# Optimization experiments

Hardware: AMD Instinct MI355X
Metric: run time of the kernel (lower is better)

Reference implementation:

```python
import jax, jax.numpy as jnp
import numpy as np

N_NODES = 50000
N_EDGES = 600000
DIM_H = 128
LN_EPS = 1e-5


def setup_inputs() -> dict:
    key = jax.random.key(0)
    ks = jax.random.split(key, 8)
    s = 1.0 / np.sqrt(DIM_H)
    return {
        "nodes": jax.random.normal(ks[0], (N_NODES, DIM_H), jnp.float32),
        "W_msg": jax.random.normal(ks[1], (DIM_H, DIM_H), jnp.float32) * s,
        "b_msg": jnp.zeros((DIM_H,), jnp.float32),
        "w_ih": jax.random.normal(ks[2], (3 * DIM_H, DIM_H), jnp.float32) * s,
        "w_hh": jax.random.normal(ks[3], (3 * DIM_H, DIM_H), jnp.float32) * s,
        "b_ih": jnp.zeros((3 * DIM_H,), jnp.float32),
        "b_hh": jnp.zeros((3 * DIM_H,), jnp.float32),
        "ln_gamma": jnp.ones((DIM_H,), jnp.float32),
        "ln_beta": jnp.zeros((DIM_H,), jnp.float32),
        "edge_src": jax.random.randint(ks[4], (N_EDGES,), 0, N_NODES, jnp.int32),
        "edge_dst": jax.random.randint(ks[5], (N_EDGES,), 0, N_NODES, jnp.int32),
    }


def _layer_norm(x, gamma, beta):
    mu = jnp.mean(x, axis=-1, keepdims=True)
    var = jnp.mean(jnp.square(x - mu), axis=-1, keepdims=True)
    return gamma * (x - mu) * jax.lax.rsqrt(var + LN_EPS) + beta


def reference(nodes, W_msg, b_msg, w_ih, w_hh, b_ih, b_hh, ln_gamma, ln_beta,
              edge_src, edge_dst):
    n_nodes = nodes.shape[0]
    # send_and_recv: per-edge message from source node, sum-reduce at dest
    msg_e = nodes[edge_src] @ W_msg.T + b_msg            # [E, H] (irregular gather)
    messages = jax.ops.segment_sum(msg_e, edge_dst, num_segments=n_nodes)  # [N, H]
    # global connection: add mean node feature
    msg = messages + jnp.mean(nodes, axis=0)
    # single-step GRU (torch gate layout: r, z, n)
    gi = msg @ w_ih.T + b_ih                             # [N, 3H]
    gh = nodes @ w_hh.T + b_hh                           # [N, 3H]
    i_r, i_z, i_n = jnp.split(gi, 3, axis=-1)
    h_r, h_z, h_n = jnp.split(gh, 3, axis=-1)
    r = jax.nn.sigmoid(i_r + h_r)
    z = jax.nn.sigmoid(i_z + h_z)
    n = jnp.tanh(i_n + r * h_n)
    h_next = (1.0 - z) * n + z * nodes
    # LayerNorm then post-GRU spatial residual with messages
    out = _layer_norm(h_next, ln_gamma, ln_beta)
    out = out + messages
    return out
```

## Files before the change

kernel.cpp:

```cpp
#include <hip/hip_runtime.h>
#include <hip/hip_bf16.h>

#define N_NODES 50000
#define N_EDGES 600000
#define DIM_H   128
#define NPAD    50048
#define NB_SCAN 196

typedef __attribute__((ext_vector_type(8))) short bf16x8;
typedef __attribute__((ext_vector_type(4))) float f32x4;
typedef __attribute__((ext_vector_type(4))) short short4v;

__device__ __forceinline__ short f2bs(float f) {
    __hip_bfloat16 h = __float2bfloat16(f);
    return *reinterpret_cast<short*>(&h);
}
__device__ __forceinline__ float bs2f(short s) {
    unsigned u = ((unsigned)(unsigned short)s) << 16;
    return __builtin_bit_cast(float, u);
}
__device__ __forceinline__ float sigm(float x) { return 1.f / (1.f + expf(-x)); }

__device__ __forceinline__ void dma16(const void* g, const void* lds_uniform) {
    __builtin_amdgcn_global_load_lds(
        (const __attribute__((address_space(1))) void*)g,
        (__attribute__((address_space(3))) void*)(unsigned)(unsigned long long)lds_uniform,
        16, 0, 0);
}

__global__ __launch_bounds__(256) void prep_k(const float* __restrict__ wmsg,
                                              const float* __restrict__ wih,
                                              const float* __restrict__ whh,
                                              short* __restrict__ wmsgB,
                                              short* __restrict__ wihB,
                                              short* __restrict__ whhB,
                                              int* __restrict__ cnt,
                                              float* __restrict__ colsum,
                                              short* __restrict__ aggTail,
                                              short* __restrict__ nodesTail,
                                              short* __restrict__ msginTail) {
    int i = blockIdx.x * 256 + threadIdx.x;
    if (i < 16384) wmsgB[i] = f2bs(wmsg[i]);
    if (i < 49152) { wihB[i] = f2bs(wih[i]); whhB[i] = f2bs(whh[i]); }
    if (i < N_NODES) cnt[i] = 0;
    if (i < 128) colsum[i] = 0.f;
    if (i < 1536) {
        short4v z = {0, 0, 0, 0};
        *(short4v*)(aggTail   + i * 4) = z;
        *(short4v*)(nodesTail + i * 4) = z;
        *(short4v*)(msginTail + i * 4) = z;
    }
}

__global__ __launch_bounds__(256) void colsum_k(const float* __restrict__ nodes,
                                                float* __restrict__ colsum,
                                                short* __restrict__ nodesB) {
    __shared__ float red[8][128];
    const int tid = threadIdx.x;
    const int cg = tid & 31;
    const int rl = tid >> 5;
    float4 acc = {0.f, 0.f, 0.f, 0.f};
    for (int r = blockIdx.x * 8 + rl; r < N_NODES; r += gridDim.x * 8) {
        float4 v = *(const float4*)(nodes + (size_t)r * DIM_H + cg * 4);
        acc.x += v.x; acc.y += v.y; acc.z += v.z; acc.w += v.w;
        *(short4v*)(nodesB + (size_t)r * DIM_H + cg * 4) =
            (short4v){f2bs(v.x), f2bs(v.y), f2bs(v.z), f2bs(v.w)};
    }
    *(float4*)&red[rl][cg * 4] = acc;
    __syncthreads();
    if (tid < 128) {
        float s = 0.f;
#pragma unroll
        for (int i = 0; i < 8; ++i) s += red[i][tid];
        unsafeAtomicAdd(&colsum[tid], s);
    }
}

__global__ __launch_bounds__(256) void hist_k(const int* __restrict__ edst,
                                              int* __restrict__ cnt) {
    int e = blockIdx.x * 256 + threadIdx.x;
    if (e < N_EDGES) atomicAdd(&cnt[edst[e]], 1);
}

__global__ __launch_bounds__(256) void bsum_k(const int* __restrict__ cnt,
                                              int* __restrict__ bsum) {
    const int t = threadIdx.x;
    int i = blockIdx.x * 256 + t;
    int v = (i < N_NODES) ? cnt[i] : 0;
#pragma unroll
    for (int o = 32; o; o >>= 1) v += __shfl_xor(v, o, 64);
    __shared__ int w4[4];
    if ((t & 63) == 0) w4[t >> 6] = v;
    __syncthreads();
    if (t == 0) bsum[blockIdx.x] = w4[0] + w4[1] + w4[2] + w4[3];
}

__global__ __launch_bounds__(256) void scan2_k(const int* __restrict__ cnt,
                                               const int* __restrict__ bsum,
                                               int* __restrict__ rowptr,
                                               int* __restrict__ pos) {
    const int b = blockIdx.x, t = threadIdx.x;
    const int lane = t & 63, w = t >> 6;
    __shared__ int red[4];
    __shared__ int wsum[4];

    int ov = (t < b) ? bsum[t] : 0;
#pragma unroll
    for (int o = 32; o; o >>= 1) ov += __shfl_xor(ov, o, 64);
    if (lane == 0) red[w] = ov;
    __syncthreads();
    const int offset = red[0] + red[1] + red[2] + red[3];

    int i = b * 256 + t;
    int v = (i < N_NODES) ? cnt[i] : 0;
    int x = v;
#pragma unroll
    for (int o = 1; o < 64; o <<= 1) {
        int y = __shfl_up(x, o, 64);
        if (lane >= o) x += y;
    }
    if (lane == 63) wsum[w] = x;
    __syncthreads();
    int woff = 0;
#pragma unroll
    for (int j = 0; j < 4; ++j)
        if (j < w) woff += wsum[j];
    int excl = offset + woff + (x - v);
    if (i < N_NODES) { rowptr[i] = excl; pos[i] = excl; }
    if (i == N_NODES - 1) rowptr[N_NODES] = excl + v;
}

__global__ __launch_bounds__(256) void reorder_k(const int* __restrict__ esrc,
                                                 const int* __restrict__ edst,
                                                 int* __restrict__ pos,
                                                 int* __restrict__ ssrc) {
    int e = blockIdx.x * 256 + threadIdx.x;
    if (e < N_EDGES) {
        int p = atomicAdd(&pos[edst[e]], 1);
        ssrc[p] = esrc[e];
    }
}

__global__ __launch_bounds__(256) void aggregate_k(const short* __restrict__ nodesB,
                                                   const int* __restrict__ rowptr,
                                                   const int* __restrict__ ssrc,
                                                   short* __restrict__ aggB) {
    const int wid = threadIdx.x >> 6;
    const int lane = threadIdx.x & 63;
    const int n = blockIdx.x * 4 + wid;
    if (n >= N_NODES) return;
    const int s0 = rowptr[n], s1 = rowptr[n + 1];
    float2 acc = {0.f, 0.f};
    int e = s0;
    for (; e + 3 < s1; e += 4) {
        int sa = ssrc[e], sb = ssrc[e + 1], sc = ssrc[e + 2], sd = ssrc[e + 3];
        short2 va = ((const short2*)(nodesB + (size_t)sa * DIM_H))[lane];
        short2 vb = ((const short2*)(nodesB + (size_t)sb * DIM_H))[lane];
        short2 vc = ((const short2*)(nodesB + (size_t)sc * DIM_H))[lane];
        short2 vd = ((const short2*)(nodesB + (size_t)sd * DIM_H))[lane];
        acc.x += (bs2f(va.x) + bs2f(vb.x)) + (bs2f(vc.x) + bs2f(vd.x));
        acc.y += (bs2f(va.y) + bs2f(vb.y)) + (bs2f(vc.y) + bs2f(vd.y));
    }
    for (; e < s1; ++e) {
        int sa = ssrc[e];
        short2 va = ((const short2*)(nodesB + (size_t)sa * DIM_H))[lane];
        acc.x += bs2f(va.x);
        acc.y += bs2f(va.y);
    }
    short2 o; o.x = f2bs(acc.x); o.y = f2bs(acc.y);
    ((short2*)(aggB + (size_t)n * DIM_H))[lane] = o;
}

__device__ __forceinline__ void stage_tile(const short* __restrict__ src, int row0,
                                           short* lds, int w, int lane) {
#pragma unroll
    for (int it = 0; it < 8; ++it) {
        int c = w * 8 + it;
        int s = c * 64 + lane;
        int r = s >> 4, q = s & 15;
        int g = q ^ (r & 15);
        dma16(src + (((size_t)(row0 + r)) << 7) + (g << 3), lds + (size_t)c * 512);
    }
}

__device__ __forceinline__ void wave_mm(const short* __restrict__ A,
                                        const short* __restrict__ W,
                                        f32x4 (&acc)[4][4],
                                        int wm, int wn, int r16, int half) {
#pragma unroll
    for (int kt = 0; kt < 4; ++kt) {
        const int sq = ((kt * 4 + half) ^ r16) << 3;
        bf16x8 af[4], bfr[4];
#pragma unroll
        for (int t = 0; t < 4; ++t) {
            af[t]  = *(const bf16x8*)&A[(wm + t * 16 + r16) * 128 + sq];
            bfr[t] = *(const bf16x8*)&W[(wn + t * 16 + r16) * 128 + sq];
        }
#pragma unroll
        for (int i = 0; i < 4; ++i)
#pragma unroll
            for (int j = 0; j < 4; ++j)
                acc[i][j] = __builtin_amdgcn_mfma_f32_16x16x32_bf16(
                    af[i], bfr[j], acc[i][j], 0, 0, 0);
    }
}

__global__ __launch_bounds__(256) void mgemm0_k(const short* __restrict__ aggB,
                                                const short* __restrict__ wmsgB,
                                                const float* __restrict__ bmsg,
                                                const int* __restrict__ degi,
                                                const float* __restrict__ colsum,
                                                short* __restrict__ msginB) {
    __shared__ short As[128 * 128];
    __shared__ short Ws[128 * 128];
    const int tid = threadIdx.x;
    const int lane = tid & 63, w = tid >> 6;
    const int m0 = blockIdx.x * 128;

    stage_tile(aggB, m0, As, w, lane);
    stage_tile(wmsgB, 0, Ws, w, lane);
    __syncthreads();

    const int r16 = lane & 15, half = lane >> 4;
    const int wm = (w >> 1) * 64, wn = (w & 1) * 64;
    f32x4 acc[4][4] = {};
    wave_mm(As, Ws, acc, wm, wn, r16, half);

#pragma unroll
    for (int i = 0; i < 4; ++i)
#pragma unroll
        for (int r = 0; r < 4; ++r) {
            int m = m0 + wm + i * 16 + half * 4 + r;
            if (m < N_NODES) {
#pragma unroll
                for (int j = 0; j < 4; ++j) {
                    int n = wn + j * 16 + r16;
                    float c = acc[i][j][r] + (float)degi[m] * bmsg[n]
                            + colsum[n] * (1.0f / N_NODES);
                    msginB[(size_t)m * 128 + n] = f2bs(c);
                }
            }
        }
}

__global__ __launch_bounds__(256) void gigh_k(const short* __restrict__ msginB,
                                              const short* __restrict__ nodesB,
                                              const short* __restrict__ wihB,
                                              const short* __restrict__ whhB,
                                              const float* __restrict__ bih,
                                              const float* __restrict__ bhh,
                                              short* __restrict__ gi,
                                              short* __restrict__ gh) {
    __shared__ short As[128 * 128];
    __shared__ short Ws[128 * 128];
    const int tid = threadIdx.x;
    const int lane = tid & 63, w = tid >> 6;
    const int m0 = blockIdx.x * 128;
    const int y = blockIdx.y;
    const short* A; const short* W; const float* bias; short* out; int n0;
    if (y < 3) { A = msginB; W = wihB; bias = bih; out = gi; n0 = y * 128; }
    else       { A = nodesB; W = whhB; bias = bhh; out = gh; n0 = (y - 3) * 128; }

    stage_tile(A, m0, As, w, lane);
    stage_tile(W, n0, Ws, w, lane);
    __syncthreads();

    const int r16 = lane & 15, half = lane >> 4;
    const int wm = (w >> 1) * 64, wn = (w & 1) * 64;
    f32x4 acc[4][4] = {};
    wave_mm(As, Ws, acc, wm, wn, r16, half);

#pragma unroll
    for (int i = 0; i < 4; ++i)
#pragma unroll
        for (int r = 0; r < 4; ++r) {
            int m = m0 + wm + i * 16 + half * 4 + r;
            if (m < N_NODES) {
#pragma unroll
                for (int j = 0; j < 4; ++j) {
                    int n = n0 + wn + j * 16 + r16;
                    out[(size_t)m * 384 + n] = f2bs(acc[i][j][r] + bias[n]);
                }
            }
        }
}

__global__ __launch_bounds__(256) void fuse_k(const short* __restrict__ nodesB,
                                              const short* __restrict__ gi,
                                              const short* __restrict__ gh,
                                              const short* __restrict__ msginB,
                                              const float* __restrict__ colsum,
                                              const float* __restrict__ gamma,
                                              const float* __restrict__ beta,
                                              float* __restrict__ out) {
    const int wid = threadIdx.x >> 6;
    const int lane = threadIdx.x & 63;
    const int n = blockIdx.x * 4 + wid;
    if (n >= N_NODES) return;

    const short* gir = gi + (size_t)n * 384;
    const short* ghr = gh + (size_t)n * 384;

    short2 ir2 = ((const short2*)gir)[lane];
    short2 iz2 = ((const short2*)(gir + 128))[lane];
    short2 in2 = ((const short2*)(gir + 256))[lane];
    short2 hr2 = ((const short2*)ghr)[lane];
    short2 hz2 = ((const short2*)(ghr + 128))[lane];
    short2 hn2 = ((const short2*)(ghr + 256))[lane];
    short2 h2  = ((const short2*)(nodesB + (size_t)n * DIM_H))[lane];
    short2 mi2 = ((const short2*)(msginB + (size_t)n * DIM_H))[lane];
    float2 cs2 = ((const float2*)colsum)[lane];
    float2 ga2 = ((const float2*)gamma)[lane];
    float2 be2 = ((const float2*)beta)[lane];

    float hn[2], resid[2];
    {
        float r = sigm(bs2f(ir2.x) + bs2f(hr2.x));
        float z = sigm(bs2f(iz2.x) + bs2f(hz2.x));
        float ng = tanhf(bs2f(in2.x) + r * bs2f(hn2.x));
        hn[0] = (1.f - z) * ng + z * bs2f(h2.x);
        resid[0] = bs2f(mi2.x) - cs2.x * (1.0f / N_NODES);
    }
    {
        float r = sigm(bs2f(ir2.y) + bs2f(hr2.y));
        float z = sigm(bs2f(iz2.y) + bs2f(hz2.y));
        float ng = tanhf(bs2f(in2.y) + r * bs2f(hn2.y));
        hn[1] = (1.f - z) * ng + z * bs2f(h2.y);
        resid[1] = bs2f(mi2.y) - cs2.y * (1.0f / N_NODES);
    }
    float s = hn[0] + hn[1];
    float q = hn[0] * hn[0] + hn[1] * hn[1];
#pragma unroll
    for (int o = 32; o; o >>= 1) {
        s += __shfl_xor(s, o, 64);
        q += __shfl_xor(q, o, 64);
    }
    float mu = s * (1.0f / DIM_H);
    float var = q * (1.0f / DIM_H) - mu * mu;
    float rstd = rsqrtf(var + 1e-5f);
    float2 o2;
    o2.x = ga2.x * (hn[0] - mu) * rstd + be2.x + resid[0];
    o2.y = ga2.y * (hn[1] - mu) * rstd + be2.y + resid[1];
    ((float2*)(out + (size_t)n * DIM_H))[lane] = o2;
}

extern "C" void kernel_launch(void* const* d_in, const int* in_sizes, int n_in,
                              void* d_out, int out_size, void* d_ws, size_t ws_size,
                              hipStream_t stream) {
    const float* nodes = (const float*)d_in[0];
    const float* Wmsg  = (const float*)d_in[1];
    const float* bmsg  = (const float*)d_in[2];
    const float* wih   = (const float*)d_in[3];
    const float* whh   = (const float*)d_in[4];
    const float* bih   = (const float*)d_in[5];
    const float* bhh   = (const float*)d_in[6];
    const float* gamma = (const float*)d_in[7];
    const float* beta  = (const float*)d_in[8];
    const int* esrc = (const int*)d_in[9];
    const int* edst = (const int*)d_in[10];
    float* out = (float*)d_out;

    char* ws = (char*)d_ws;
    short* gi_s   = (short*)ws;
    short* gh_s   = (short*)(ws + 38400000);
    short* aggB   = (short*)(ws + 76800000);
    short* nodesB = (short*)(ws + 89612288);
    short* msginB = (short*)(ws + 102424576);
    short* wmsgB  = (short*)(ws + 115236864);
    short* wihB   = (short*)(ws + 115269632);
    short* whhB   = (short*)(ws + 115367936);
    float* colsum = (float*)(ws + 115466240);
    int*   cnt    = (int*)(ws + 115466752);
    int*   rowptr = (int*)(ws + 115666752);
    int*   pos    = (int*)(ws + 115866760);
    int*   ssrc   = (int*)(ws + 116066760);
    int*   bsum   = (int*)(ws + 118466760);

    short* aggTail   = aggB   + (size_t)N_NODES * DIM_H;
    short* nodesTail = nodesB + (size_t)N_NODES * DIM_H;
    short* msginTail = msginB + (size_t)N_NODES * DIM_H;

    prep_k<<<NB_SCAN, 256, 0, stream>>>(Wmsg, wih, whh, wmsgB, wihB, whhB,
                                        cnt, colsum, aggTail, nodesTail, msginTail);
    colsum_k<<<512, 256, 0, stream>>>(nodes, colsum, nodesB);

    const int EB = (N_EDGES + 255) / 256;
    hist_k<<<EB, 256, 0, stream>>>(edst, cnt);
    bsum_k<<<NB_SCAN, 256, 0, stream>>>(cnt, bsum);
    scan2_k<<<NB_SCAN, 256, 0, stream>>>(cnt, bsum, rowptr, pos);
    reorder_k<<<EB, 256, 0, stream>>>(esrc, edst, pos, ssrc);
    aggregate_k<<<(N_NODES + 3) / 4, 256, 0, stream>>>(nodesB, rowptr, ssrc, aggB);

    const int MB2 = (N_NODES + 127) / 128;
    mgemm0_k<<<dim3(MB2, 1), 256, 0, stream>>>(aggB, wmsgB, bmsg, cnt, colsum, msginB);
    gigh_k<<<dim3(MB2, 6), 256, 0, stream>>>(msginB, nodesB, wihB, whhB, bih, bhh,
                                             gi_s, gh_s);

    fuse_k<<<(N_NODES + 3) / 4, 256, 0, stream>>>(nodesB, gi_s, gh_s, msginB,
                                                  colsum, gamma, beta, out);
}
```

Before: 268.5 us.

## Fuse message GEMM, GRU gate GEMMs, and LayerNorm into one kernel

```diff
diff --git a/kernel.cpp b/kernel.cpp
--- a/kernel.cpp
+++ b/kernel.cpp
@@ -19,7 +19,15 @@
     unsigned u = ((unsigned)(unsigned short)s) << 16;
     return __builtin_bit_cast(float, u);
 }
-__device__ __forceinline__ float sigm(float x) { return 1.f / (1.f + expf(-x)); }
+__device__ __forceinline__ float sigm(float x) { return 1.f / (1.f + __expf(-x)); }
+__device__ __forceinline__ float tanh_f(float x) {
+    return 2.f / (1.f + __expf(-2.f * x)) - 1.f;
+}
+__device__ __forceinline__ unsigned pk2(float a, float b) {
+    return ((unsigned)(unsigned short)f2bs(b) << 16) | (unsigned)(unsigned short)f2bs(a);
+}
+__device__ __forceinline__ float unlo(unsigned u) { return bs2f((short)(u & 0xffffu)); }
+__device__ __forceinline__ float unhi(unsigned u) { return bs2f((short)(u >> 16)); }
 
 __device__ __forceinline__ void dma16(const void* g, const void* lds_uniform) {
     __builtin_amdgcn_global_load_lds(
@@ -37,8 +45,7 @@
                                               int* __restrict__ cnt,
                                               float* __restrict__ colsum,
                                               short* __restrict__ aggTail,
-                                              short* __restrict__ nodesTail,
-                                              short* __restrict__ msginTail) {
+                                              short* __restrict__ nodesTail) {
     int i = blockIdx.x * 256 + threadIdx.x;
     if (i < 16384) wmsgB[i] = f2bs(wmsg[i]);
     if (i < 49152) { wihB[i] = f2bs(wih[i]); whhB[i] = f2bs(whh[i]); }
@@ -48,7 +55,6 @@
         short4v z = {0, 0, 0, 0};
         *(short4v*)(aggTail   + i * 4) = z;
         *(short4v*)(nodesTail + i * 4) = z;
-        *(short4v*)(msginTail + i * 4) = z;
     }
 }
 
@@ -183,18 +189,19 @@
     }
 }
 
-__device__ __forceinline__ void wave_mm(const short* __restrict__ A,
-                                        const short* __restrict__ W,
-                                        f32x4 (&acc)[4][4],
-                                        int wm, int wn, int r16, int half) {
+__device__ __forceinline__ void wave_mm_g(const short* __restrict__ A,
+                                          const short* __restrict__ Wg,
+                                          f32x4 (&acc)[4][4],
+                                          int wm, int wn, int r16, int half) {
 #pragma unroll
     for (int kt = 0; kt < 4; ++kt) {
-        const int sq = ((kt * 4 + half) ^ r16) << 3;
+        const int kg = kt * 4 + half;
+        const int sq = (kg ^ r16) << 3;
         bf16x8 af[4], bfr[4];
 #pragma unroll
         for (int t = 0; t < 4; ++t) {
             af[t]  = *(const bf16x8*)&A[(wm + t * 16 + r16) * 128 + sq];
-            bfr[t] = *(const bf16x8*)&W[(wn + t * 16 + r16) * 128 + sq];
+            bfr[t] = *(const bf16x8*)(Wg + (size_t)(wn + t * 16 + r16) * 128 + (kg << 3));
         }
 #pragma unroll
         for (int i = 0; i < 4; ++i)
@@ -205,143 +212,205 @@
     }
 }
 
-__global__ __launch_bounds__(256) void mgemm0_k(const short* __restrict__ aggB,
-                                                const short* __restrict__ wmsgB,
-                                                const float* __restrict__ bmsg,
-                                                const int* __restrict__ degi,
-                                                const float* __restrict__ colsum,
-                                                short* __restrict__ msginB) {
-    __shared__ short As[128 * 128];
-    __shared__ short Ws[128 * 128];
+#define ZACC()                                        \
+    _Pragma("unroll") for (int i = 0; i < 4; ++i)     \
+    _Pragma("unroll") for (int j = 0; j < 4; ++j)     \
+        acc[i][j] = (f32x4){0.f, 0.f, 0.f, 0.f}
+
+__global__ __launch_bounds__(256) void fused_k(const short* __restrict__ aggB,
+                                               const short* __restrict__ nodesB,
+                                               const short* __restrict__ wmsgB,
+                                               const short* __restrict__ wihB,
+                                               const short* __restrict__ whhB,
+                                               const float* __restrict__ bmsg,
+                                               const float* __restrict__ bih,
+                                               const float* __restrict__ bhh,
+                                               const int* __restrict__ deg,
+                                               const float* __restrict__ colsum,
+                                               const float* __restrict__ gamma,
+                                               const float* __restrict__ beta,
+                                               float* __restrict__ out) {
+    __shared__ short Ms[128 * 128];
+    __shared__ short Ns[128 * 128];
+    __shared__ float redS[128][2];
+    __shared__ float redQ[128][2];
+
     const int tid = threadIdx.x;
     const int lane = tid & 63, w = tid >> 6;
     const int m0 = blockIdx.x * 128;
-
-    stage_tile(aggB, m0, As, w, lane);
-    stage_tile(wmsgB, 0, Ws, w, lane);
-    __syncthreads();
-
     const int r16 = lane & 15, half = lane >> 4;
     const int wm = (w >> 1) * 64, wn = (w & 1) * 64;
-    f32x4 acc[4][4] = {};
-    wave_mm(As, Ws, acc, wm, wn, r16, half);
+    const float invN = 1.0f / N_NODES;
+
+    stage_tile(aggB, m0, Ms, w, lane);
+    stage_tile(nodesB, m0, Ns, w, lane);
+    __syncthreads();
+
+    f32x4 acc[4][4];
+
+    ZACC();
+    wave_mm_g(Ms, wmsgB, acc, wm, wn, r16, half);
+    __syncthreads();
+    {
+        float bm[4], cs[4];
+#pragma unroll
+        for (int j = 0; j < 4; ++j) {
+            int c = wn + j * 16 + r16;
+            bm[j] = bmsg[c];
+            cs[j] = colsum[c] * invN;
+        }
+#pragma unroll
+        for (int i = 0; i < 4; ++i)
+#pragma unroll
+            for (int rr = 0; rr < 4; ++rr) {
+                int lr = wm + i * 16 + half * 4 + rr;
+                int gm = m0 + lr;
+                float dg = (gm < N_NODES) ? (float)deg[gm] : 0.f;
+#pragma unroll
+                for (int j = 0; j < 4; ++j) {
+                    int c = wn + j * 16 + r16;
+                    float v = acc[i][j][rr] + dg * bm[j] + cs[j];
+                    int slot = (c >> 3) ^ (lr & 15);
+                    Ms[lr * 128 + slot * 8 + (c & 7)] = f2bs(v);
+                }
+            }
+    }
+    __syncthreads();
+
+    unsigned hnp[4][4][2];
+    {
+        ZACC();
+        wave_mm_g(Ns, whhB + 256 * 128, acc, wm, wn, r16, half);
+        float bh[4];
+#pragma unroll
+        for (int j = 0; j < 4; ++j) bh[j] = bhh[256 + wn + j * 16 + r16];
+#pragma unroll
+        for (int i = 0; i < 4; ++i)
+#pragma unroll
+            for (int j = 0; j < 4; ++j) {
+                hnp[i][j][0] = pk2(acc[i][j][0] + bh[j], acc[i][j][1] + bh[j]);
+                hnp[i][j][1] = pk2(acc[i][j][2] + bh[j], acc[i][j][3] + bh[j]);
+            }
+    }
+
+    unsigned rp[4][4][2];
+    {
+        ZACC();
+        wave_mm_g(Ms, wihB, acc, wm, wn, r16, half);
+        wave_mm_g(Ns, whhB, acc, wm, wn, r16, half);
+        float b0[4];
+#pragma unroll
+        for (int j = 0; j < 4; ++j) {
+            int c = wn + j * 16 + r16;
+            b0[j] = bih[c] + bhh[c];
+        }
+#pragma unroll
+        for (int i = 0; i < 4; ++i)
+#pragma unroll
+            for (int j = 0; j < 4; ++j) {
+                rp[i][j][0] = pk2(sigm(acc[i][j][0] + b0[j]), sigm(acc[i][j][1] + b0[j]));
+                rp[i][j][1] = pk2(sigm(acc[i][j][2] + b0[j]), sigm(acc[i][j][3] + b0[j]));
+            }
+    }
+
+    unsigned np[4][4][2];
+    {
+        ZACC();
+        wave_mm_g(Ms, wihB + 256 * 128, acc, wm, wn, r16, half);
+        float bi[4];
+#pragma unroll
+        for (int j = 0; j < 4; ++j) bi[j] = bih[256 + wn + j * 16 + r16];
+#pragma unroll
+        for (int i = 0; i < 4; ++i)
+#pragma unroll
+            for (int j = 0; j < 4; ++j) {
+                float n0 = tanh_f(acc[i][j][0] + bi[j] + unlo(rp[i][j][0]) * unlo(hnp[i][j][0]));
+                float n1 = tanh_f(acc[i][j][1] + bi[j] + unhi(rp[i][j][0]) * unhi(hnp[i][j][0]));
+                float n2 = tanh_f(acc[i][j][2] + bi[j] + unlo(rp[i][j][1]) * unlo(hnp[i][j][1]));
+                float n3 = tanh_f(acc[i][j][3] + bi[j] + unhi(rp[i][j][1]) * unhi(hnp[i][j][1]));
+                np[i][j][0] = pk2(n0, n1);
+                np[i][j][1] = pk2(n2, n3);
+            }
+    }
+
+    {
+        ZACC();
+        wave_mm_g(Ms, wihB + 128 * 128, acc, wm, wn, r16, half);
+        wave_mm_g(Ns, whhB + 128 * 128, acc, wm, wn, r16, half);
+        float b1[4];
+#pragma unroll
+        for (int j = 0; j < 4; ++j) {
+            int c = wn + j * 16 + r16;
+            b1[j] = bih[128 + c] + bhh[128 + c];
+        }
+#pragma unroll
+        for (int i = 0; i < 4; ++i)
+#pragma unroll
+            for (int j = 0; j < 4; ++j)
+#pragma unroll
+                for (int rr = 0; rr < 4; ++rr) {
+                    int lr = wm + i * 16 + half * 4 + rr;
+                    int c = wn + j * 16 + r16;
+                    int slot = (c >> 3) ^ (lr & 15);
+                    float h = bs2f(Ns[lr * 128 + slot * 8 + (c & 7)]);
+                    float z = sigm(acc[i][j][rr] + b1[j]);
+                    float nv = (rr & 1) ? unhi(np[i][j][rr >> 1]) : unlo(np[i][j][rr >> 1]);
+                    acc[i][j][rr] = (1.f - z) * nv + z * h;
+                }
+    }
 
 #pragma unroll
     for (int i = 0; i < 4; ++i)
 #pragma unroll
-        for (int r = 0; r < 4; ++r) {
-            int m = m0 + wm + i * 16 + half * 4 + r;
-            if (m < N_NODES) {
-#pragma unroll
-                for (int j = 0; j < 4; ++j) {
-                    int n = wn + j * 16 + r16;
-                    float c = acc[i][j][r] + (float)degi[m] * bmsg[n]
-                            + colsum[n] * (1.0f / N_NODES);
-                    msginB[(size_t)m * 128 + n] = f2bs(c);
+        for (int rr = 0; rr < 4; ++rr) {
+            float s = acc[i][0][rr] + acc[i][1][rr] + acc[i][2][rr] + acc[i][3][rr];
+            float q = acc[i][0][rr] * acc[i][0][rr] + acc[i][1][rr] * acc[i][1][rr]
+                    + acc[i][2][rr] * acc[i][2][rr] + acc[i][3][rr] * acc[i][3][rr];
+#pragma unroll
+            for (int o = 1; o < 16; o <<= 1) {
+                s += __shfl_xor(s, o, 64);
+                q += __shfl_xor(q, o, 64);
+            }
+            if (r16 == 0) {
+                int lr = wm + i * 16 + half * 4 + rr;
+                redS[lr][wn >> 6] = s;
+                redQ[lr][wn >> 6] = q;
+            }
+        }
+    __syncthreads();
+
+    {
+        float ga[4], be[4], cs[4];
+#pragma unroll
+        for (int j = 0; j < 4; ++j) {
+            int c = wn + j * 16 + r16;
+            ga[j] = gamma[c];
+            be[j] = beta[c];
+            cs[j] = colsum[c] * invN;
+        }
+#pragma unroll
+        for (int i = 0; i < 4; ++i)
+#pragma unroll
+            for (int rr = 0; rr < 4; ++rr) {
+                int lr = wm + i * 16 + half * 4 + rr;
+                int gm = m0 + lr;
+                float S = redS[lr][0] + redS[lr][1];
+                float Q = redQ[lr][0] + redQ[lr][1];
+                float mu = S * (1.0f / DIM_H);
+                float var = Q * (1.0f / DIM_H) - mu * mu;
+                float rstd = rsqrtf(var + 1e-5f);
+                if (gm < N_NODES) {
+#pragma unroll
+                    for (int j = 0; j < 4; ++j) {
+                        int c = wn + j * 16 + r16;
+                        int slot = (c >> 3) ^ (lr & 15);
+                        float resid = bs2f(Ms[lr * 128 + slot * 8 + (c & 7)]) - cs[j];
+                        out[(size_t)gm * DIM_H + c] =
+                            ga[j] * (acc[i][j][rr] - mu) * rstd + be[j] + resid;
+                    }
                 }
             }
-        }
-}
-
-__global__ __launch_bounds__(256) void gigh_k(const short* __restrict__ msginB,
-                                              const short* __restrict__ nodesB,
-                                              const short* __restrict__ wihB,
-                                              const short* __restrict__ whhB,
-                                              const float* __restrict__ bih,
-                                              const float* __restrict__ bhh,
-                                              short* __restrict__ gi,
-                                              short* __restrict__ gh) {
-    __shared__ short As[128 * 128];
-    __shared__ short Ws[128 * 128];
-    const int tid = threadIdx.x;
-    const int lane = tid & 63, w = tid >> 6;
-    const int m0 = blockIdx.x * 128;
-    const int y = blockIdx.y;
-    const short* A; const short* W; const float* bias; short* out; int n0;
-    if (y < 3) { A = msginB; W = wihB; bias = bih; out = gi; n0 = y * 128; }
-    else       { A = nodesB; W = whhB; bias = bhh; out = gh; n0 = (y - 3) * 128; }
-
-    stage_tile(A, m0, As, w, lane);
-    stage_tile(W, n0, Ws, w, lane);
-    __syncthreads();
-
-    const int r16 = lane & 15, half = lane >> 4;
-    const int wm = (w >> 1) * 64, wn = (w & 1) * 64;
-    f32x4 acc[4][4] = {};
-    wave_mm(As, Ws, acc, wm, wn, r16, half);
-
-#pragma unroll
-    for (int i = 0; i < 4; ++i)
-#pragma unroll
-        for (int r = 0; r < 4; ++r) {
-            int m = m0 + wm + i * 16 + half * 4 + r;
-            if (m < N_NODES) {
-#pragma unroll
-                for (int j = 0; j < 4; ++j) {
-                    int n = n0 + wn + j * 16 + r16;
-                    out[(size_t)m * 384 + n] = f2bs(acc[i][j][r] + bias[n]);
-                }
-            }
-        }
-}
-
-__global__ __launch_bounds__(256) void fuse_k(const short* __restrict__ nodesB,
-                                              const short* __restrict__ gi,
-                                              const short* __restrict__ gh,
-                                              const short* __restrict__ msginB,
-                                              const float* __restrict__ colsum,
-                                              const float* __restrict__ gamma,
-                                              const float* __restrict__ beta,
-                                              float* __restrict__ out) {
-    const int wid = threadIdx.x >> 6;
-    const int lane = threadIdx.x & 63;
-    const int n = blockIdx.x * 4 + wid;
-    if (n >= N_NODES) return;
-
-    const short* gir = gi + (size_t)n * 384;
-    const short* ghr = gh + (size_t)n * 384;
-
-    short2 ir2 = ((const short2*)gir)[lane];
-    short2 iz2 = ((const short2*)(gir + 128))[lane];
-    short2 in2 = ((const short2*)(gir + 256))[lane];
-    short2 hr2 = ((const short2*)ghr)[lane];
-    short2 hz2 = ((const short2*)(ghr + 128))[lane];
-    short2 hn2 = ((const short2*)(ghr + 256))[lane];
-    short2 h2  = ((const short2*)(nodesB + (size_t)n * DIM_H))[lane];
-    short2 mi2 = ((const short2*)(msginB + (size_t)n * DIM_H))[lane];
-    float2 cs2 = ((const float2*)colsum)[lane];
-    float2 ga2 = ((const float2*)gamma)[lane];
-    float2 be2 = ((const float2*)beta)[lane];
-
-    float hn[2], resid[2];
-    {
-        float r = sigm(bs2f(ir2.x) + bs2f(hr2.x));
-        float z = sigm(bs2f(iz2.x) + bs2f(hz2.x));
-        float ng = tanhf(bs2f(in2.x) + r * bs2f(hn2.x));
-        hn[0] = (1.f - z) * ng + z * bs2f(h2.x);
-        resid[0] = bs2f(mi2.x) - cs2.x * (1.0f / N_NODES);
-    }
-    {
-        float r = sigm(bs2f(ir2.y) + bs2f(hr2.y));
-        float z = sigm(bs2f(iz2.y) + bs2f(hz2.y));
-        float ng = tanhf(bs2f(in2.y) + r * bs2f(hn2.y));
-        hn[1] = (1.f - z) * ng + z * bs2f(h2.y);
-        resid[1] = bs2f(mi2.y) - cs2.y * (1.0f / N_NODES);
-    }
-    float s = hn[0] + hn[1];
-    float q = hn[0] * hn[0] + hn[1] * hn[1];
-#pragma unroll
-    for (int o = 32; o; o >>= 1) {
-        s += __shfl_xor(s, o, 64);
-        q += __shfl_xor(q, o, 64);
-    }
-    float mu = s * (1.0f / DIM_H);
-    float var = q * (1.0f / DIM_H) - mu * mu;
-    float rstd = rsqrtf(var + 1e-5f);
-    float2 o2;
-    o2.x = ga2.x * (hn[0] - mu) * rstd + be2.x + resid[0];
-    o2.y = ga2.y * (hn[1] - mu) * rstd + be2.y + resid[1];
-    ((float2*)(out + (size_t)n * DIM_H))[lane] = o2;
+    }
 }
 
 extern "C" void kernel_launch(void* const* d_in, const int* in_sizes, int n_in,
@@ -361,27 +430,23 @@
     float* out = (float*)d_out;
 
     char* ws = (char*)d_ws;
-    short* gi_s   = (short*)ws;
-    short* gh_s   = (short*)(ws + 38400000);
-    short* aggB   = (short*)(ws + 76800000);
-    short* nodesB = (short*)(ws + 89612288);
-    short* msginB = (short*)(ws + 102424576);
-    short* wmsgB  = (short*)(ws + 115236864);
-    short* wihB   = (short*)(ws + 115269632);
-    short* whhB   = (short*)(ws + 115367936);
-    float* colsum = (float*)(ws + 115466240);
-    int*   cnt    = (int*)(ws + 115466752);
-    int*   rowptr = (int*)(ws + 115666752);
-    int*   pos    = (int*)(ws + 115866760);
-    int*   ssrc   = (int*)(ws + 116066760);
-    int*   bsum   = (int*)(ws + 118466760);
+    short* aggB   = (short*)ws;
+    short* nodesB = (short*)(ws + 12812288);
+    short* wmsgB  = (short*)(ws + 25624576);
+    short* wihB   = (short*)(ws + 25657344);
+    short* whhB   = (short*)(ws + 25755648);
+    float* colsum = (float*)(ws + 25853952);
+    int*   cnt    = (int*)(ws + 25854464);
+    int*   rowptr = (int*)(ws + 26054464);
+    int*   pos    = (int*)(ws + 26254480);
+    int*   ssrc   = (int*)(ws + 26454480);
+    int*   bsum   = (int*)(ws + 28854480);
 
     short* aggTail   = aggB   + (size_t)N_NODES * DIM_H;
     short* nodesTail = nodesB + (size_t)N_NODES * DIM_H;
-    short* msginTail = msginB + (size_t)N_NODES * DIM_H;
 
     prep_k<<<NB_SCAN, 256, 0, stream>>>(Wmsg, wih, whh, wmsgB, wihB, whhB,
-                                        cnt, colsum, aggTail, nodesTail, msginTail);
+                                        cnt, colsum, aggTail, nodesTail);
     colsum_k<<<512, 256, 0, stream>>>(nodes, colsum, nodesB);
 
     const int EB = (N_EDGES + 255) / 256;
@@ -392,10 +457,6 @@
     aggregate_k<<<(N_NODES + 3) / 4, 256, 0, stream>>>(nodesB, rowptr, ssrc, aggB);
 
     const int MB2 = (N_NODES + 127) / 128;
-    mgemm0_k<<<dim3(MB2, 1), 256, 0, stream>>>(aggB, wmsgB, bmsg, cnt, colsum, msginB);
-    gigh_k<<<dim3(MB2, 6), 256, 0, stream>>>(msginB, nodesB, wihB, whhB, bih, bhh,
-                                             gi_s, gh_s);
-
-    fuse_k<<<(N_NODES + 3) / 4, 256, 0, stream>>>(nodesB, gi_s, gh_s, msginB,
-                                                  colsum, gamma, beta, out);
-}
+    fused_k<<<MB2, 256, 0, stream>>>(aggB, nodesB, wmsgB, wihB, whhB,
+                                     bmsg, bih, bhh, cnt, colsum, gamma, beta, out);
+}
```

New measurement: 308.1 us. +14.7%, slower.
